# Kernel tuning notes

Hardware: AMD Instinct MI355X
Metric: run time of the kernel (lower is better)

## Reference

```python
import jax, jax.numpy as jnp
import numpy as np
import math

# dims
B, C, T, P = 32, 8, 20000, 25          # batch, emg channels, time, patch size
D, H, M, NL = 512, 8, 256, 2            # d_model, heads, random features, layers
FFN, NC, HID = 1024, 10, 128            # ffn hidden, num classes, pool hidden
DH = D // H                             # d_head
EPS_LN = 1e-5


def _sample_omega(d, m, rng):
    # Orthogonal Random Features: blocks of QR(G) rows scaled by chi(d) norms
    blocks = []
    for _ in range(math.ceil(m / d)):
        G = rng.standard_normal((d, d)).astype(np.float32)
        Q, _ = np.linalg.qr(G)
        S = Q * np.linalg.norm(G, axis=1, keepdims=True)
        blocks.append(S.T)
    return np.concatenate(blocks, axis=1)[:, :m]


def setup_inputs() -> dict:
    key = jax.random.key(0)
    ks = jax.random.split(key, 16)
    rng = np.random.default_rng(0)
    s = 0.02
    f32 = jnp.float32
    return {
        "x": jax.random.normal(ks[0], (B, C, T), f32),
        "patch_W": jax.random.normal(ks[1], (C * P, D), f32) * s,
        "patch_b": jnp.zeros((D,), f32),
        "patch_g": jnp.ones((D,), f32),
        "patch_beta": jnp.zeros((D,), f32),
        "ln1_g": jnp.ones((NL, D), f32),
        "ln1_b": jnp.zeros((NL, D), f32),
        "qW": jax.random.normal(ks[2], (NL, D, D), f32) * s,
        "kW": jax.random.normal(ks[3], (NL, D, D), f32) * s,
        "vW": jax.random.normal(ks[4], (NL, D, D), f32) * s,
        "oW": jax.random.normal(ks[5], (NL, D, D), f32) * s,
        "ob": jnp.zeros((NL, D), f32),
        "omega": jnp.stack([jnp.asarray(_sample_omega(DH, M, rng)) for _ in range(NL)]),
        "ln2_g": jnp.ones((NL, D), f32),
        "ln2_b": jnp.zeros((NL, D), f32),
        "f1W": jax.random.normal(ks[6], (NL, D, FFN), f32) * s,
        "f1b": jnp.zeros((NL, FFN), f32),
        "f2W": jax.random.normal(ks[7], (NL, FFN, D), f32) * s,
        "f2b": jnp.zeros((NL, D), f32),
        "poolW1": jax.random.normal(ks[8], (D, HID), f32) * s,
        "poolW2": jax.random.normal(ks[9], (HID, 1), f32) * s,
        "headW": jax.random.normal(ks[10], (2 * D, NC), f32) * s,
        "headb": jnp.zeros((NC,), f32),
    }


def _ln(x, g, b):
    mu = jnp.mean(x, -1, keepdims=True)
    v = jnp.mean((x - mu) ** 2, -1, keepdims=True)
    return (x - mu) / jnp.sqrt(v + EPS_LN) * g + b


def _phi(x, omega):
    # FAVOR+ positive feature map: exp(x'w / d^{1/4} - |x|^2/(2 sqrt(d))) / sqrt(m)
    xs = x / (DH ** 0.25)                               # (B,H,L,d)
    proj = jnp.einsum('bhld,dm->bhlm', xs, omega)       # (B,H,L,m)
    nsq = 0.5 * jnp.sum(xs * xs, -1, keepdims=True)
    return jnp.exp(proj - nsq) / (M ** 0.5)


def _attn(x, qW, kW, vW, oW, ob, omega):
    Bx, L, _ = x.shape
    Q = (x @ qW).reshape(Bx, L, H, DH).transpose(0, 2, 1, 3)
    K = (x @ kW).reshape(Bx, L, H, DH).transpose(0, 2, 1, 3)
    V = (x @ vW).reshape(Bx, L, H, DH).transpose(0, 2, 1, 3)
    Qf = _phi(Q, omega)
    Kf = _phi(K, omega)
    KV = jnp.einsum('bhlm,bhld->bhmd', Kf, V)           # O(L m d)
    out = jnp.einsum('bhlm,bhmd->bhld', Qf, KV)
    norm = jnp.einsum('bhlm,bhm->bhl', Qf, Kf.sum(2))[..., None]
    out = out / jnp.maximum(norm, 1e-6)
    out = out.transpose(0, 2, 1, 3).reshape(Bx, L, D)
    return out @ oW + ob


def _forward(x, patch_W, patch_b, patch_g, patch_beta, ln1_g, ln1_b, qW, kW, vW,
             oW, ob, omega, ln2_g, ln2_b, f1W, f1b, f2W, f2b, poolW1, poolW2,
             headW, headb):
    Bx, Cx, Tx = x.shape
    pad = (-Tx) % P
    if pad:
        x = jnp.pad(x, ((0, 0), (0, 0), (0, pad)))
    L = x.shape[2] // P
    # patchify: (B,C,T)->(B,L,C*P) then linear + LN
    tok = x.reshape(Bx, Cx, L, P).transpose(0, 2, 1, 3).reshape(Bx, L, Cx * P)
    h = _ln(tok @ patch_W + patch_b, patch_g, patch_beta)
    for l in range(NL):  # pre-LN performer layers (dropout = eval mode)
        h = h + _attn(_ln(h, ln1_g[l], ln1_b[l]), qW[l], kW[l], vW[l], oW[l], ob[l], omega[l])
        z = _ln(h, ln2_g[l], ln2_b[l])
        h = h + (jax.nn.gelu(z @ f1W[l] + f1b[l], approximate=False) @ f2W[l] + f2b[l])
    # attentive statistics pooling over tokens
    alpha = jax.nn.softmax(jnp.tanh(h @ poolW1) @ poolW2, axis=1)  # (B,L,1)
    mu = jnp.sum(alpha * h, axis=1)
    var = jnp.sum(alpha * h * h, axis=1) - mu * mu
    feat = jnp.concatenate([mu, jnp.sqrt(jnp.clip(var, 1e-8))], axis=1)
    return feat @ headW + headb  # (B, NC)


def reference(x, patch_W, patch_b, patch_g, patch_beta, ln1_g, ln1_b, qW, kW, vW,
              oW, ob, omega, ln2_g, ln2_b, f1W, f1b, f2W, f2b, poolW1, poolW2,
              headW, headb):
    return _forward(x, patch_W, patch_b, patch_g, patch_beta, ln1_g, ln1_b, qW,
                    kW, vW, oW, ob, omega, ln2_g, ln2_b, f1W, f1b, f2W, f2b,
                    poolW1, poolW2, headW, headb)
```

## Files before the change

kernel.cpp:

```cpp
#include <hip/hip_runtime.h>
#include <math.h>

#define BB 32
#define CC 8
#define TT 20000
#define PP 25
#define LL 800
#define CP 200
#define DD 512
#define HH 8
#define MM 256
#define NLAYER 2
#define DHH 64
#define FF 1024
#define NCLS 10
#define HIDP 128
#define BL (BB*LL)
#define KPATCH 256

#define WT_PATCH 0
#define WT_QKV0  131072
#define WT_OW0   917504
#define WT_F10   1179648
#define WT_F20   1703936
#define WT_QKV1  2228224
#define WT_OW1   3014656
#define WT_F11   3276800
#define WT_F21   3801088
#define WT_POOL  4325376
#define WT_TOTAL 4390912
#define NUC 5120

typedef unsigned short u16;
typedef unsigned int u32;
typedef __attribute__((ext_vector_type(8))) short short8;
typedef __attribute__((ext_vector_type(4))) float f32x4;

__device__ __forceinline__ float b2f(u16 v) { return __uint_as_float(((u32)v) << 16); }
__device__ __forceinline__ float b2f_lo(u32 u) { return __uint_as_float(u << 16); }
__device__ __forceinline__ float b2f_hi(u32 u) { return __uint_as_float(u & 0xFFFF0000u); }
__device__ __forceinline__ u16 f2b(float f) {
  u32 u = __float_as_uint(f);
  u32 r = u + 0x7FFFu + ((u >> 16) & 1u);
  return (u16)(r >> 16);
}
__device__ __forceinline__ float ldx(const void* p, size_t i, int flag) {
  return flag ? b2f(((const u16*)p)[i]) : ((const float*)p)[i];
}
typedef const __attribute__((address_space(1))) u32 gas_u32;
typedef __attribute__((address_space(3))) u32 las_u32;
__device__ __forceinline__ void gload16(const void* g, void* l) {
  __builtin_amdgcn_global_load_lds((gas_u32*)(size_t)g, (las_u32*)(size_t)l, 16, 0, 0);
}

__global__ void sniff_kernel(const u32* __restrict__ g, u32* __restrict__ flagp) {
  if (threadIdx.x == 0) flagp[0] = (g[0] == 0x3F800000u) ? 0u : 1u;
}

__global__ void sentinel_kernel(u16* out, int n) {
  int i = blockIdx.x * 256 + threadIdx.x;
  if (i < n) out[i] = f2b(1.0e9f);
}

__global__ void patchify_kernel(const void* __restrict__ x, u16* __restrict__ tok,
                                const u32* __restrict__ dflag) {
  int flag = (int)dflag[0];
  int idx = blockIdx.x * 256 + threadIdx.x;
  if (idx >= BL * KPATCH) return;
  int col = idx & (KPATCH - 1), row = idx >> 8;
  if (col >= CP) { tok[idx] = 0; return; }
  int b = row / LL, l = row % LL;
  int c = col / PP, p = col % PP;
  tok[idx] = f2b(ldx(x, ((size_t)b * CC + c) * TT + l * PP + p, flag));
}

__global__ void omcvt_kernel(const void* __restrict__ om, u16* __restrict__ ombT,
                             const u32* __restrict__ dflag) {
  int flag = (int)dflag[0];
  const float inv4 = 0.35355339059327373f;
  int idx = blockIdx.x * 256 + threadIdx.x;
  if (idx >= NLAYER * MM * DHH) return;
  int l = idx >> 14;
  int r = idx & (MM * DHH - 1);
  int feat = r >> 6, k = r & 63;
  ombT[idx] = f2b(inv4 * ldx(om, (size_t)l * DHH * MM + (size_t)k * MM + feat, flag));
}

struct Seg { int t0, wsel, gsel, woff, goff, wtoff, ucoff, K, N, Kp; };
__constant__ Seg g_segs[14] = {
  {   0, 0, -1,      0,   0, WT_PATCH,          -1,  200,  512,  256},
  {  32, 2,  0,      0,   0, WT_QKV0,             0,  512,  512,  512},
  {  96, 3,  0,      0,   0, WT_QKV0 + 262144,  512,  512,  512,  512},
  { 160, 1,  0,      0,   0, WT_QKV0 + 524288, 1024,  512,  512,  512},
  { 224, 4, -1,      0,   0, WT_OW0,            -1,  512,  512,  512},
  { 288, 5,  1,      0,   0, WT_F10,           1536,  512, 1024,  512},
  { 416, 6, -1,      0,   0, WT_F20,            -1, 1024,  512, 1024},
  { 544, 2,  0, 262144, 512, WT_QKV1,          2560,  512,  512,  512},
  { 608, 3,  0, 262144, 512, WT_QKV1 + 262144, 3072,  512,  512,  512},
  { 672, 1,  0, 262144, 512, WT_QKV1 + 524288, 3584,  512,  512,  512},
  { 736, 4, -1, 262144,   0, WT_OW1,            -1,  512,  512,  512},
  { 800, 5,  1, 524288, 512, WT_F11,           4096,  512, 1024,  512},
  { 928, 6, -1, 524288,   0, WT_F21,            -1, 1024,  512, 1024},
  {1056, 7, -1,      0,   0, WT_POOL,           -1,  512,  128,  512},
};

__global__ __launch_bounds__(256) void megawt_kernel(
    const void* __restrict__ patchW, const void* __restrict__ qW,
    const void* __restrict__ kW, const void* __restrict__ vW,
    const void* __restrict__ oW, const void* __restrict__ f1W,
    const void* __restrict__ f2W, const void* __restrict__ poolW1,
    const void* __restrict__ ln1g, const void* __restrict__ ln1b,
    const void* __restrict__ ln2g, const void* __restrict__ ln2b,
    u16* __restrict__ wtall, float* __restrict__ pU, float* __restrict__ pC,
    const u32* __restrict__ dflag) {
  int flag = (int)dflag[0];
  int bid = blockIdx.x;
  int si = 0;
#pragma unroll
  for (int i = 1; i < 14; i++) if (bid >= g_segs[i].t0) si = i;
  Seg sg = g_segs[si];
  const void* W = (sg.wsel == 0) ? patchW : (sg.wsel == 1) ? qW : (sg.wsel == 2) ? kW
               : (sg.wsel == 3) ? vW : (sg.wsel == 4) ? oW : (sg.wsel == 5) ? f1W
               : (sg.wsel == 6) ? f2W : poolW1;
  const void* gv = (sg.gsel == 0) ? ln1g : (sg.gsel == 1) ? ln2g : nullptr;
  const void* bv = (sg.gsel == 0) ? ln1b : (sg.gsel == 1) ? ln2b : nullptr;
  int lt = bid - sg.t0;
  int nx = sg.N >> 6;
  int n0 = (lt % nx) * 64, k0 = (lt / nx) * 64;
  bool hasU = sg.ucoff >= 0;

  __shared__ float tile[64][65];
  __shared__ float sU[4][64], sC[4][64];
  int tn = threadIdx.x & 63;
  int tk = threadIdx.x >> 6;
  float su = 0.f, sc = 0.f;
#pragma unroll 4
  for (int i = 0; i < 16; i++) {
    int k = k0 + tk * 16 + i;
    float gw = 0.f;
    if (k < sg.K) {
      float w = ldx(W, (size_t)sg.woff + (size_t)k * sg.N + n0 + tn, flag);
      float g = gv ? ldx(gv, (size_t)sg.goff + k, flag) : 1.0f;
      gw = g * w;
      if (hasU) {
        su += gw;
        sc = fmaf(ldx(bv, (size_t)sg.goff + k, flag), w, sc);
      }
    }
    tile[tk * 16 + i][tn] = gw;
  }
  if (hasU) { sU[tk][tn] = su; sC[tk][tn] = sc; }
  __syncthreads();
  if (hasU && tk == 0) {
    pU[(size_t)(k0 >> 6) * NUC + sg.ucoff + n0 + tn] =
        sU[0][tn] + sU[1][tn] + sU[2][tn] + sU[3][tn];
    pC[(size_t)(k0 >> 6) * NUC + sg.ucoff + n0 + tn] =
        sC[0][tn] + sC[1][tn] + sC[2][tn] + sC[3][tn];
  }
#pragma unroll 4
  for (int i = 0; i < 16; i++) {
    int n = n0 + tk * 16 + i;
    wtall[(size_t)sg.wtoff + (size_t)n * sg.Kp + k0 + tn] = f2b(tile[tn][tk * 16 + i]);
  }
}

__global__ __launch_bounds__(256) void ucr_kernel(const float* __restrict__ pU,
    const float* __restrict__ pC, float* __restrict__ u, float* __restrict__ c, int N) {
  int n = blockIdx.x * 256 + threadIdx.x;
  if (n >= N) return;
  float su = 0.f, sc = 0.f;
#pragma unroll
  for (int ky = 0; ky < 8; ky++) {
    su += pU[(size_t)ky * N + n];
    sc += pC[(size_t)ky * N + n];
  }
  u[n] = su;
  c[n] = sc;
}

template<int ACT, bool HAS_BIAS, bool HAS_RES, int LNE, bool SPLIT3, bool STATS>
__global__ __launch_bounds__(256, 4) void mgemm(
    const u16* __restrict__ A, const u16* __restrict__ Wt,
    const void* __restrict__ bias, size_t biasoff,
    const float* __restrict__ stA, const float* __restrict__ stB,
    const float* __restrict__ uvec, const float* __restrict__ cvec,
    const u16* res, u16* out, u16* out2, u16* out3,
    float* __restrict__ oSum, float* __restrict__ oSsq,
    int Kp, int N, const u32* __restrict__ dflag) {
  const int flag = (int)dflag[0];
  alignas(16) __shared__ u16 smem[128 * 128];
  __shared__ float statL[256];
  u16* As = smem;
  u16* Bs = smem + 128 * 64;
  int tid = threadIdx.x;
  int flat = blockIdx.y * gridDim.x + blockIdx.x;
  int xcd = flat & 7;
  int p_ = flat >> 3;
  int gx = gridDim.x;
  int mtile = xcd * (gridDim.y >> 3) + p_ / gx;
  int ntile = p_ % gx;
  int m0 = mtile * 128, n0 = ntile * 128;
  int wid = tid >> 6, lane = tid & 63;
  int wm = (wid >> 1) * 64, wn = (wid & 1) * 64;
  int quad = lane >> 4, cl = lane & 15;

  if (LNE == 1) {
    if (tid < 128) {
      statL[tid] = stA[m0 + tid];
      statL[128 + tid] = stB[m0 + tid];
    }
  } else if (LNE == 2) {
    if (tid < 128) {
      float s = 0.f, q = 0.f;
#pragma unroll
      for (int s8 = 0; s8 < 8; s8++) {
        s += stA[(size_t)s8 * BL + m0 + tid];
        q += stB[(size_t)s8 * BL + m0 + tid];
      }
      float mu = s * (1.f / DD);
      float var = q * (1.f / DD) - mu * mu;
      statL[tid] = mu;
      statL[128 + tid] = 1.0f / sqrtf(var + 1e-5f);
    }
  }

  f32x4 acc[4][4] = {};
  int r_ = tid >> 3, c_ = tid & 7;
  for (int k0 = 0; k0 < Kp; k0 += 64) {
    __syncthreads();
#pragma unroll
    for (int p = 0; p < 4; p++) {
      int row = p * 32 + r_;
      int gc = (c_ ^ (row & 7)) * 8;
      int lbase = ((p * 256 + (tid & ~63)) * 8);
      gload16(A + (size_t)(m0 + row) * Kp + k0 + gc, &As[lbase]);
      gload16(Wt + (size_t)(n0 + row) * Kp + k0 + gc, &Bs[lbase]);
    }
    __syncthreads();
#pragma unroll
    for (int kk = 0; kk < 64; kk += 32) {
      int qb = (kk >> 3) + quad;
      short8 af[4], bf[4];
#pragma unroll
      for (int mt = 0; mt < 4; mt++) {
        int arow = wm + mt * 16 + cl;
        af[mt] = *(const short8*)(&As[(arow * 8 + (qb ^ (cl & 7))) * 8]);
      }
#pragma unroll
      for (int nt = 0; nt < 4; nt++) {
        int brow = wn + nt * 16 + cl;
        bf[nt] = *(const short8*)(&Bs[(brow * 8 + (qb ^ (cl & 7))) * 8]);
      }
#pragma unroll
      for (int mt = 0; mt < 4; mt++)
#pragma unroll
        for (int nt = 0; nt < 4; nt++)
          acc[mt][nt] = __builtin_amdgcn_mfma_f32_16x16x32_bf16(
              af[mt], bf[nt], acc[mt][nt], 0, 0, 0);
    }
  }
  __syncthreads();
  u16* Cs = smem;
  float sA[4][4] = {}, qA[4][4] = {};
#pragma unroll
  for (int nt = 0; nt < 4; nt++) {
    int tcol = wn + nt * 16 + cl;
    int gcol = n0 + tcol;
    float bvv = HAS_BIAS ? ldx(bias, biasoff + gcol, flag) : 0.f;
    float uv_ = 0.f, cv_ = 0.f;
    if (LNE) { uv_ = uvec[gcol]; cv_ = cvec[gcol]; }
#pragma unroll
    for (int mt = 0; mt < 4; mt++) {
#pragma unroll
      for (int r = 0; r < 4; r++) {
        int trow = wm + mt * 16 + quad * 4 + r;
        int grow = m0 + trow;
        float v = acc[mt][nt][r];
        if (LNE) {
          float rv_ = statL[128 + trow];
          v = rv_ * v - rv_ * statL[trow] * uv_ + cv_;
        }
        v += bvv;
        if (ACT == 1) v = 0.5f * v * (1.0f + erff(v * 0.7071067811865476f));
        else if (ACT == 2) v = tanhf(v);
        if (HAS_RES) v += b2f(res[(size_t)grow * N + gcol]);
        u16 wv = f2b(v);
        Cs[trow * 128 + tcol] = wv;
        if (STATS) {
          float vr = b2f(wv);
          sA[mt][r] += vr;
          qA[mt][r] += vr * vr;
        }
      }
    }
  }
  if (STATS) {
#pragma unroll
    for (int mt = 0; mt < 4; mt++)
#pragma unroll
      for (int r = 0; r < 4; r++) {
        float s = sA[mt][r], q = qA[mt][r];
        s += __shfl_xor(s, 1, 64); s += __shfl_xor(s, 2, 64);
        s += __shfl_xor(s, 4, 64); s += __shfl_xor(s, 8, 64);
        q += __shfl_xor(q, 1, 64); q += __shfl_xor(q, 2, 64);
        q += __shfl_xor(q, 4, 64); q += __shfl_xor(q, 8, 64);
        if (cl == 0) {
          int grow = m0 + wm + mt * 16 + quad * 4 + r;
          int slot = ntile * 2 + (wid & 1);
          oSum[(size_t)slot * BL + grow] = s;
          oSsq[(size_t)slot * BL + grow] = q;
        }
      }
  }
  __syncthreads();
  {
    u16* dstbuf;
    int colbase, stride;
    if (SPLIT3) {
      int sel = n0 >> 9;
      dstbuf = (sel == 0) ? out : (sel == 1) ? out2 : out3;
      colbase = n0 & 511;
      stride = 512;
    } else {
      dstbuf = out;
      colbase = n0;
      stride = N;
    }
    int c8 = (tid & 15) * 8, rb = tid >> 4;
#pragma unroll
    for (int i = 0; i < 8; i++) {
      int trow = i * 16 + rb;
      uint4 vv = *(const uint4*)(&Cs[trow * 128 + c8]);
      *(uint4*)(&dstbuf[(size_t)(m0 + trow) * stride + colbase + c8]) = vv;
    }
  }
}

__global__ __launch_bounds__(256) void ln_apply_kernel(const u16* __restrict__ x,
    const float* __restrict__ pSum, const float* __restrict__ pSsq,
    const void* __restrict__ g, const void* __restrict__ b, u16* __restrict__ out,
    float* __restrict__ muv, float* __restrict__ rinvv,
    const u32* __restrict__ dflag) {
  int flag = (int)dflag[0];
  int row = blockIdx.x * 4 + (threadIdx.x >> 6);
  int lane = threadIdx.x & 63;
  float s = 0.f, q = 0.f;
#pragma unroll
  for (int s8 = 0; s8 < 8; s8++) {
    s += pSum[(size_t)s8 * BL + row];
    q += pSsq[(size_t)s8 * BL + row];
  }
  float m = s * (1.f / DD);
  float var = q * (1.f / DD) - m * m;
  float rvv = 1.0f / sqrtf(var + 1e-5f);

  const u16* xr = x + (size_t)row * DD + lane * 8;
  uint4 u = *(const uint4*)xr;
  float f[8] = {b2f_lo(u.x), b2f_hi(u.x), b2f_lo(u.y), b2f_hi(u.y),
                b2f_lo(u.z), b2f_hi(u.z), b2f_lo(u.w), b2f_hi(u.w)};
  u16 r[8];
  float os = 0.f, oq = 0.f;
#pragma unroll
  for (int j = 0; j < 8; j++) {
    float gg = ldx(g, lane * 8 + j, flag);
    float bb = ldx(b, lane * 8 + j, flag);
    r[j] = f2b((f[j] - m) * rvv * gg + bb);
    float hv = b2f(r[j]);
    os += hv;
    oq = fmaf(hv, hv, oq);
  }
  uint4 pr;
  pr.x = (u32)r[0] | ((u32)r[1] << 16);
  pr.y = (u32)r[2] | ((u32)r[3] << 16);
  pr.z = (u32)r[4] | ((u32)r[5] << 16);
  pr.w = (u32)r[6] | ((u32)r[7] << 16);
  *(uint4*)(out + (size_t)row * DD + lane * 8) = pr;
#pragma unroll
  for (int o = 1; o < 64; o <<= 1) {
    os += __shfl_xor(os, o, 64);
    oq += __shfl_xor(oq, o, 64);
  }
  if (lane == 0) {
    float mo = os * (1.f / DD);
    float vo = oq * (1.f / DD) - mo * mo;
    muv[row] = mo;
    rinvv[row] = 1.0f / sqrtf(vo + 1e-5f);
  }
}

__global__ __launch_bounds__(256) void kv_kernel_mfma(
    const u16* __restrict__ Kb, const u16* __restrict__ Vb,
    const u16* __restrict__ omt, u16* __restrict__ KVT_g) {
  int bh = blockIdx.x; int b = bh >> 3, h = bh & 7;
  int tid = threadIdx.x;
  int wid = tid >> 6, lane = tid & 63;
  int quad = lane >> 4, cl = lane & 15;
  __shared__ u16 VT[80 * 40];
  __shared__ u16 KfT[256 * 40];

  short8 omB[4][2];
#pragma unroll
  for (int nt = 0; nt < 4; nt++)
#pragma unroll
    for (int ks = 0; ks < 2; ks++)
      omB[nt][ks] = *(const short8*)(omt + (size_t)(wid * 64 + nt * 16 + cl) * 64
                                         + ks * 32 + quad * 8);
  for (int e = tid; e < 512; e += 256)
    VT[(64 + (e >> 5)) * 40 + (e & 31)] = ((e >> 5) == 0) ? (u16)0x3F80 : (u16)0;

  f32x4 acc2[4][5] = {};

  for (int l0 = 0; l0 < LL; l0 += 32) {
    __syncthreads();
#pragma unroll
    for (int i = 0; i < 4; i++) {
      int idx = tid + i * 256;
      int rr = idx >> 5, pp = idx & 31;
      u32 uv = *(const u32*)(Vb + ((size_t)(b * LL + l0 + rr)) * DD + h * DHH + pp * 2);
      VT[(pp * 2) * 40 + rr] = (u16)(uv & 0xFFFF);
      VT[(pp * 2 + 1) * 40 + rr] = (u16)(uv >> 16);
    }
    short8 aK[2][2];
    float nsk[2];
#pragma unroll
    for (int mt = 0; mt < 2; mt++) {
      const u16* ksrc = Kb + ((size_t)(b * LL + l0 + mt * 16 + cl)) * DD + h * DHH;
#pragma unroll
      for (int ks = 0; ks < 2; ks++)
        aK[mt][ks] = *(const short8*)(ksrc + ks * 32 + quad * 8);
      float q = 0.f;
#pragma unroll
      for (int ks = 0; ks < 2; ks++)
#pragma unroll
        for (int j = 0; j < 8; j++) {
          float f = b2f((u16)aK[mt][ks][j]);
          q = fmaf(f, f, q);
        }
      q += __shfl_xor(q, 16, 64);
      q += __shfl_xor(q, 32, 64);
      nsk[mt] = 0.0625f * q;
    }
    f32x4 acc1[2][4] = {};
#pragma unroll
    for (int ks = 0; ks < 2; ks++)
#pragma unroll
      for (int mt = 0; mt < 2; mt++)
#pragma unroll
        for (int nt = 0; nt < 4; nt++)
          acc1[mt][nt] = __builtin_amdgcn_mfma_f32_16x16x32_bf16(
              aK[mt][ks], omB[nt][ks], acc1[mt][nt], 0, 0, 0);
#pragma unroll
    for (int mt = 0; mt < 2; mt++) {
      f32x4 nsv;
#pragma unroll
      for (int r = 0; r < 4; r++) nsv[r] = __shfl(nsk[mt], quad * 4 + r, 64);
#pragma unroll
      for (int nt = 0; nt < 4; nt++) {
        int m = wid * 64 + nt * 16 + cl;
        u16 kf16[4];
#pragma unroll
        for (int r = 0; r < 4; r++)
          kf16[r] = f2b(__expf(acc1[mt][nt][r] - nsv[r]) * 0.0625f);
        uint2 pk;
        pk.x = (u32)kf16[0] | ((u32)kf16[1] << 16);
        pk.y = (u32)kf16[2] | ((u32)kf16[3] << 16);
        *(uint2*)(&KfT[m * 40 + mt * 16 + quad * 4]) = pk;
      }
    }
    __syncthreads();
    short8 aF[4], bV[5];
#pragma unroll
    for (int mt2 = 0; mt2 < 4; mt2++)
      aF[mt2] = *(const short8*)(&KfT[(wid * 64 + mt2 * 16 + cl) * 40 + quad * 8]);
#pragma unroll
    for (int nt2 = 0; nt2 < 5; nt2++)
      bV[nt2] = *(const short8*)(&VT[(nt2 * 16 + cl) * 40 + quad * 8]);
#pragma unroll
    for (int mt2 = 0; mt2 < 4; mt2++)
#pragma unroll
      for (int nt2 = 0; nt2 < 5; nt2++)
        acc2[mt2][nt2] = __builtin_amdgcn_mfma_f32_16x16x32_bf16(
            aF[mt2], bV[nt2], acc2[mt2][nt2], 0, 0, 0);
  }
  u16* base = KVT_g + (size_t)bh * 80 * 256;
#pragma unroll
  for (int mt2 = 0; mt2 < 4; mt2++) {
    int m0 = wid * 64 + mt2 * 16 + quad * 4;
#pragma unroll
    for (int nt2 = 0; nt2 < 4; nt2++) {
      u16 w[4];
#pragma unroll
      for (int r = 0; r < 4; r++) w[r] = f2b(acc2[mt2][nt2][r]);
      uint2 pk;
      pk.x = (u32)w[0] | ((u32)w[1] << 16);
      pk.y = (u32)w[2] | ((u32)w[3] << 16);
      *(uint2*)(&base[(size_t)(nt2 * 16 + cl) * 256 + m0]) = pk;
    }
    if (cl == 0) {
      u16 w[4];
#pragma unroll
      for (int r = 0; r < 4; r++) w[r] = f2b(acc2[mt2][4][r]);
      uint2 pk;
      pk.x = (u32)w[0] | ((u32)w[1] << 16);
      pk.y = (u32)w[2] | ((u32)w[3] << 16);
      *(uint2*)(&base[(size_t)64 * 256 + m0]) = pk;
    }
  }
}

__global__ __launch_bounds__(256) void attn_out_mfma(
    u16* __restrict__ Qb, const u16* __restrict__ KVT_g,
    const u16* __restrict__ omt) {
  int bh = blockIdx.x; int b = bh >> 3, h = bh & 7;
  int chunk = blockIdx.y;
  int tid = threadIdx.x;
  int wid = tid >> 6, lane = tid & 63;
  int quad = lane >> 4, cl = lane & 15;
  __shared__ u16 smem[64 * 264 + 80 * 264];
  u16* Qf = smem;
  u16* KVT = smem + 64 * 264;

  const u16* kvsrc = KVT_g + (size_t)bh * 80 * 256;
#pragma unroll
  for (int i = 0; i < 9; i++) {
    int idx = tid + i * 256;
    if (idx < 2080) {
      int row = idx >> 5, c8 = (idx & 31) * 8;
      *(uint4*)(&KVT[row * 264 + c8]) = *(const uint4*)(kvsrc + (size_t)row * 256 + c8);
    }
  }

  short8 omB[4][2];
#pragma unroll
  for (int nt = 0; nt < 4; nt++)
#pragma unroll
    for (int ks = 0; ks < 2; ks++)
      omB[nt][ks] = *(const short8*)(omt + (size_t)(wid * 64 + nt * 16 + cl) * 64
                                         + ks * 32 + quad * 8);

  int t0 = chunk * 64;
  short8 aQ[4][2];
  float nss[4];
#pragma unroll
  for (int mt = 0; mt < 4; mt++) {
    int tglob = t0 + mt * 16 + cl;
    int trow = tglob < LL ? tglob : LL - 1;
    const u16* qsrc = Qb + ((size_t)(b * LL + trow)) * DD + h * DHH;
#pragma unroll
    for (int ks = 0; ks < 2; ks++)
      aQ[mt][ks] = *(const short8*)(qsrc + ks * 32 + quad * 8);
    float q = 0.f;
#pragma unroll
    for (int ks = 0; ks < 2; ks++)
#pragma unroll
      for (int j = 0; j < 8; j++) {
        float f = b2f((u16)aQ[mt][ks][j]);
        q = fmaf(f, f, q);
      }
    q += __shfl_xor(q, 16, 64);
    q += __shfl_xor(q, 32, 64);
    nss[mt] = 0.0625f * q;
  }

  f32x4 acc1[4][4] = {};
#pragma unroll
  for (int ks = 0; ks < 2; ks++)
#pragma unroll
    for (int mt = 0; mt < 4; mt++)
#pragma unroll
      for (int nt = 0; nt < 4; nt++)
        acc1[mt][nt] = __builtin_amdgcn_mfma_f32_16x16x32_bf16(
            omB[nt][ks], aQ[mt][ks], acc1[mt][nt], 0, 0, 0);
#pragma unroll
  for (int mt = 0; mt < 4; mt++) {
#pragma unroll
    for (int nt = 0; nt < 4; nt++) {
      u16 w[4];
#pragma unroll
      for (int r = 0; r < 4; r++)
        w[r] = f2b(__expf(acc1[mt][nt][r] - nss[mt]) * 0.0625f);
      uint2 pk;
      pk.x = (u32)w[0] | ((u32)w[1] << 16);
      pk.y = (u32)w[2] | ((u32)w[3] << 16);
      *(uint2*)(&Qf[(mt * 16 + cl) * 264 + wid * 64 + nt * 16 + quad * 4]) = pk;
    }
  }
  __syncthreads();
  f32x4 acc2[5] = {};
#pragma unroll
  for (int ks2 = 0; ks2 < 8; ks2++) {
    short8 aF = *(const short8*)(&Qf[(wid * 16 + cl) * 264 + ks2 * 32 + quad * 8]);
#pragma unroll
    for (int nt2 = 0; nt2 < 5; nt2++) {
      short8 bK = *(const short8*)(&KVT[(nt2 * 16 + cl) * 264 + ks2 * 32 + quad * 8]);
      acc2[nt2] = __builtin_amdgcn_mfma_f32_16x16x32_bf16(bK, aF, acc2[nt2], 0, 0, 0);
    }
  }
  float nval = __shfl(acc2[4][0], cl, 64);
  float inv = 1.0f / fmaxf(nval, 1e-6f);
  int tglob = t0 + wid * 16 + cl;
  if (tglob < LL) {
    u16* dst = Qb + ((size_t)(b * LL + tglob)) * DD + h * DHH;
#pragma unroll
    for (int nt2 = 0; nt2 < 4; nt2++) {
      u16 w[4];
#pragma unroll
      for (int r = 0; r < 4; r++) w[r] = f2b(acc2[nt2][r] * inv);
      uint2 pk;
      pk.x = (u32)w[0] | ((u32)w[1] << 16);
      pk.y = (u32)w[2] | ((u32)w[3] << 16);
      *(uint2*)(dst + nt2 * 16 + quad * 4) = pk;
    }
  }
}

__global__ __launch_bounds__(256) void score_kernel(const u16* __restrict__ t,
    const void* __restrict__ w2, float* __restrict__ sc, const u32* __restrict__ dflag) {
  int flag = (int)dflag[0];
  int row = blockIdx.x * 4 + (threadIdx.x >> 6);
  int lane = threadIdx.x & 63;
  const u16* tr = t + (size_t)row * HIDP;
  float p = b2f(tr[lane]) * ldx(w2, lane, flag) +
            b2f(tr[lane + 64]) * ldx(w2, lane + 64, flag);
#pragma unroll
  for (int o = 32; o; o >>= 1) p += __shfl_down(p, o, 64);
  if (lane == 0) sc[row] = p;
}

__global__ __launch_bounds__(256) void softmax_kernel(const float* __restrict__ sc,
    float* __restrict__ alpha) {
  __shared__ float sm[4];
  int b = blockIdx.x, tid = threadIdx.x;
  float mx = -1e30f;
  for (int i = tid; i < LL; i += 256) mx = fmaxf(mx, sc[b * LL + i]);
#pragma unroll
  for (int o = 32; o; o >>= 1) mx = fmaxf(mx, __shfl_down(mx, o, 64));
  if ((tid & 63) == 0) sm[tid >> 6] = mx;
  __syncthreads();
  mx = fmaxf(fmaxf(sm[0], sm[1]), fmaxf(sm[2], sm[3]));
  float s = 0.f;
  for (int i = tid; i < LL; i += 256) {
    float e = expf(sc[b * LL + i] - mx);
    alpha[b * LL + i] = e;
    s += e;
  }
  __syncthreads();
#pragma unroll
  for (int o = 32; o; o >>= 1) s += __shfl_down(s, o, 64);
  if ((tid & 63) == 0) sm[tid >> 6] = s;
  __syncthreads();
  float invs = 1.f / (sm[0] + sm[1] + sm[2] + sm[3]);
  for (int i = tid; i < LL; i += 256) alpha[b * LL + i] *= invs;
}

__global__ __launch_bounds__(512) void pool_stats_kernel(const u16* __restrict__ h,
    const float* __restrict__ alpha, float* __restrict__ feat) {
  int b = blockIdx.x, d = threadIdx.x;
  float mu = 0.f, m2 = 0.f;
  const u16* hb = h + (size_t)b * LL * DD + d;
  const float* ab = alpha + b * LL;
  for (int l = 0; l < LL; l++) {
    float a = ab[l], v = b2f(hb[(size_t)l * DD]);
    mu = fmaf(a, v, mu);
    m2 = fmaf(a * v, v, m2);
  }
  feat[b * 2 * DD + d] = mu;
  float var = m2 - mu * mu;
  feat[b * 2 * DD + DD + d] = sqrtf(fmaxf(var, 1e-8f));
}

__global__ __launch_bounds__(320) void head_kernel(const float* __restrict__ feat,
    const void* __restrict__ hw, const void* __restrict__ hb, void* out,
    const u32* __restrict__ dflag) {
  int flag = (int)dflag[0];
  int b = blockIdx.x;
  int t = threadIdx.x;
  int n = t >> 5, j0 = t & 31;
  float p = 0.f;
  for (int j = j0; j < 2 * DD; j += 32)
    p = fmaf(feat[b * 2 * DD + j], ldx(hw, (size_t)j * NCLS + n, flag), p);
#pragma unroll
  for (int o = 16; o; o >>= 1) p += __shfl_down(p, o, 32);
  if (j0 == 0) {
    float v = p + ldx(hb, n, flag);
    if (flag) ((u16*)out)[b * NCLS + n] = f2b(v);
    else ((float*)out)[b * NCLS + n] = v;
  }
}

extern "C" void kernel_launch(void* const* d_in, const int* in_sizes, int n_in,
                              void* d_out, int out_size, void* d_ws, size_t ws_size,
                              hipStream_t stream) {
  char* ws = (char*)d_ws;
  size_t off = 0;
  auto alloc = [&](size_t bytes) -> char* {
    char* p = ws + off;
    off += (bytes + 255) & ~(size_t)255;
    return p;
  };
  u16* hbuf = (u16*)alloc((size_t)BL * DD * 2);
  u16* buf1 = (u16*)alloc((size_t)BL * DD * 2);
  u16* buf2 = (u16*)alloc((size_t)BL * DD * 2);
  u16* KVT_g = (u16*)alloc((size_t)BB * HH * 80 * 256 * 2);
  float* muv = (float*)alloc((size_t)BL * 4);
  float* rinvv = (float*)alloc((size_t)BL * 4);
  float* scores = (float*)alloc((size_t)BL * 4);
  float* alpha = (float*)alloc((size_t)BL * 4);
  float* feat = (float*)alloc((size_t)BB * 2 * DD * 4);
  float* uvec = (float*)alloc((size_t)NUC * 4);
  float* cvec = (float*)alloc((size_t)NUC * 4);
  float* pU = (float*)alloc((size_t)8 * NUC * 4);
  float* pC = (float*)alloc((size_t)8 * NUC * 4);
  float* pSum = (float*)alloc((size_t)8 * BL * 4);
  float* pSsq = (float*)alloc((size_t)8 * BL * 4);
  u16* ombT = (u16*)alloc((size_t)NLAYER * MM * DHH * 2);
  u16* wtall = (u16*)alloc((size_t)WT_TOTAL * 2);
  u32* dflag = (u32*)alloc(256);
  size_t off_base = off;
  u16* bufQ = (u16*)alloc((size_t)BL * DD * 2);
  size_t off_full = off;

  if (ws_size < off_base) {
    sentinel_kernel<<<2, 256, 0, stream>>>((u16*)d_out, out_size);
    return;
  }
  const bool fused = (ws_size >= off_full);

  const void* x       = d_in[0];
  const void* patchW  = d_in[1];
  const void* patchb  = d_in[2];
  const void* patchg  = d_in[3];
  const void* patchbe = d_in[4];
  const void* ln1g    = d_in[5];
  const void* ln1b    = d_in[6];
  const void* qW      = d_in[7];
  const void* kW      = d_in[8];
  const void* vW      = d_in[9];
  const void* oW      = d_in[10];
  const void* ob      = d_in[11];
  const void* omg     = d_in[12];
  const void* ln2g    = d_in[13];
  const void* ln2b    = d_in[14];
  const void* f1W     = d_in[15];
  const void* f1b     = d_in[16];
  const void* f2W     = d_in[17];
  const void* f2b_    = d_in[18];
  const void* poolW1  = d_in[19];
  const void* poolW2  = d_in[20];
  const void* headW   = d_in[21];
  const void* headb   = d_in[22];

  sniff_kernel<<<1, 64, 0, stream>>>((const u32*)patchg, dflag);

  patchify_kernel<<<(BL * KPATCH) / 256, 256, 0, stream>>>(x, buf1, dflag);
  omcvt_kernel<<<(NLAYER * MM * DHH + 255) / 256, 256, 0, stream>>>(omg, ombT, dflag);
  megawt_kernel<<<1072, 256, 0, stream>>>(patchW, qW, kW, vW, oW, f1W, f2W, poolW1,
                                          ln1g, ln1b, ln2g, ln2b, wtall, pU, pC, dflag);
  ucr_kernel<<<NUC / 256, 256, 0, stream>>>(pU, pC, uvec, cvec, NUC);

  mgemm<0, true, false, 0, false, true><<<dim3(4, 200), 256, 0, stream>>>(
      buf1, wtall + WT_PATCH, patchb, 0, nullptr, nullptr, nullptr, nullptr,
      nullptr, buf2, nullptr, nullptr, pSum, pSsq, KPATCH, DD, dflag);
  ln_apply_kernel<<<BL / 4, 256, 0, stream>>>(buf2, pSum, pSsq, patchg, patchbe,
                                              hbuf, muv, rinvv, dflag);

  for (int l = 0; l < NLAYER; l++) {
    size_t oD = (size_t)l * DD;
    size_t oF = (size_t)l * FF;
    const u16* omtl = ombT + (size_t)l * MM * DHH;
    const u16* qkvT = wtall + (l == 0 ? WT_QKV0 : WT_QKV1);
    const u16* oWT  = wtall + (l == 0 ? WT_OW0 : WT_OW1);
    const u16* f1T  = wtall + (l == 0 ? WT_F10 : WT_F11);
    const u16* f2T  = wtall + (l == 0 ? WT_F20 : WT_F21);
    const float* uq = uvec + (l == 0 ? 0 : 2560);
    const float* cq = cvec + (l == 0 ? 0 : 2560);
    const float* uf = uvec + (l == 0 ? 1536 : 4096);
    const float* cf = cvec + (l == 0 ? 1536 : 4096);

    u16* qb;
    if (fused) {
      if (l == 0)
        mgemm<0, false, false, 1, true, false><<<dim3(12, 200), 256, 0, stream>>>(
            hbuf, qkvT, nullptr, 0, muv, rinvv, uq, cq, nullptr,
            buf1, buf2, bufQ, nullptr, nullptr, DD, 3 * DD, dflag);
      else
        mgemm<0, false, false, 2, true, false><<<dim3(12, 200), 256, 0, stream>>>(
            hbuf, qkvT, nullptr, 0, pSum, pSsq, uq, cq, nullptr,
            buf1, buf2, bufQ, nullptr, nullptr, DD, 3 * DD, dflag);
      kv_kernel_mfma<<<BB * HH, 256, 0, stream>>>(buf1, buf2, omtl, KVT_g);
      qb = bufQ;
    } else {
      if (l == 0) {
        mgemm<0, false, false, 1, false, false><<<dim3(4, 200), 256, 0, stream>>>(
            hbuf, qkvT, nullptr, 0, muv, rinvv, uq, cq, nullptr,
            buf1, nullptr, nullptr, nullptr, nullptr, DD, DD, dflag);
        mgemm<0, false, false, 1, false, false><<<dim3(4, 200), 256, 0, stream>>>(
            hbuf, qkvT + 262144, nullptr, 0, muv, rinvv, uq + 512, cq + 512, nullptr,
            buf2, nullptr, nullptr, nullptr, nullptr, DD, DD, dflag);
      } else {
        mgemm<0, false, false, 2, false, false><<<dim3(4, 200), 256, 0, stream>>>(
            hbuf, qkvT, nullptr, 0, pSum, pSsq, uq, cq, nullptr,
            buf1, nullptr, nullptr, nullptr, nullptr, DD, DD, dflag);
        mgemm<0, false, false, 2, false, false><<<dim3(4, 200), 256, 0, stream>>>(
            hbuf, qkvT + 262144, nullptr, 0, pSum, pSsq, uq + 512, cq + 512, nullptr,
            buf2, nullptr, nullptr, nullptr, nullptr, DD, DD, dflag);
      }
      kv_kernel_mfma<<<BB * HH, 256, 0, stream>>>(buf1, buf2, omtl, KVT_g);
      if (l == 0)
        mgemm<0, false, false, 1, false, false><<<dim3(4, 200), 256, 0, stream>>>(
            hbuf, qkvT + 524288, nullptr, 0, muv, rinvv, uq + 1024, cq + 1024, nullptr,
            buf1, nullptr, nullptr, nullptr, nullptr, DD, DD, dflag);
      else
        mgemm<0, false, false, 2, false, false><<<dim3(4, 200), 256, 0, stream>>>(
            hbuf, qkvT + 524288, nullptr, 0, pSum, pSsq, uq + 1024, cq + 1024, nullptr,
            buf1, nullptr, nullptr, nullptr, nullptr, DD, DD, dflag);
      qb = buf1;
    }
    attn_out_mfma<<<dim3(BB * HH, 13), 256, 0, stream>>>(qb, KVT_g, omtl);
    mgemm<0, true, true, 0, false, true><<<dim3(4, 200), 256, 0, stream>>>(
        qb, oWT, ob, oD, nullptr, nullptr, nullptr, nullptr,
        hbuf, hbuf, nullptr, nullptr, pSum, pSsq, DD, DD, dflag);
    mgemm<1, true, false, 2, false, false><<<dim3(8, 200), 256, 0, stream>>>(
        hbuf, f1T, f1b, oF, pSum, pSsq, uf, cf, nullptr,
        buf1, nullptr, nullptr, nullptr, nullptr, DD, FF, dflag);
    if (l == 0)
      mgemm<0, true, true, 0, false, true><<<dim3(4, 200), 256, 0, stream>>>(
          buf1, f2T, f2b_, oD, nullptr, nullptr, nullptr, nullptr,
          hbuf, hbuf, nullptr, nullptr, pSum, pSsq, FF, DD, dflag);
    else
      mgemm<0, true, true, 0, false, false><<<dim3(4, 200), 256, 0, stream>>>(
          buf1, f2T, f2b_, oD, nullptr, nullptr, nullptr, nullptr,
          hbuf, hbuf, nullptr, nullptr, nullptr, nullptr, FF, DD, dflag);
  }

  mgemm<2, false, false, 0, false, false><<<dim3(1, 200), 256, 0, stream>>>(
      hbuf, wtall + WT_POOL, nullptr, 0, nullptr, nullptr, nullptr, nullptr,
      nullptr, buf1, nullptr, nullptr, nullptr, nullptr, DD, HIDP, dflag);
  score_kernel<<<BL / 4, 256, 0, stream>>>(buf1, poolW2, scores, dflag);
  softmax_kernel<<<BB, 256, 0, stream>>>(scores, alpha);
  pool_stats_kernel<<<BB, 512, 0, stream>>>(hbuf, alpha, feat);
  head_kernel<<<BB, 320, 0, stream>>>(feat, headW, headb, d_out, dflag);
}
```

Before: 904.3 us.

## Merge prep kernels, prefetch V in kv kernel, split pooling, coarsen attn_out

Folds the patchify, omega conversion and weight prep kernels into a single launch to cut launch overhead. The kv kernel now register-prefetches the next V tile so the global load overlaps the MFMA work. attn_out processes two 64-token chunks per block, launching 7 y-blocks instead of 13. Pooling statistics are split across 8 segments per batch and then reduced, so many more blocks run than the previous 32. Together these trade a few extra registers and one extra tiny kernel for more parallelism and fewer launches.

```diff
diff --git a/kernel.cpp b/kernel.cpp
--- a/kernel.cpp
+++ b/kernel.cpp
@@ -31,6 +31,10 @@
 #define WT_TOTAL 4390912
 #define NUC 5120
 
+#define PREP_MEGA 1072
+#define PREP_OM   1200
+#define PREP_TOT  26800
+
 typedef unsigned short u16;
 typedef unsigned int u32;
 typedef __attribute__((ext_vector_type(8))) short short8;
@@ -60,30 +64,6 @@
 __global__ void sentinel_kernel(u16* out, int n) {
   int i = blockIdx.x * 256 + threadIdx.x;
   if (i < n) out[i] = f2b(1.0e9f);
-}
-
-__global__ void patchify_kernel(const void* __restrict__ x, u16* __restrict__ tok,
-                                const u32* __restrict__ dflag) {
-  int flag = (int)dflag[0];
-  int idx = blockIdx.x * 256 + threadIdx.x;
-  if (idx >= BL * KPATCH) return;
-  int col = idx & (KPATCH - 1), row = idx >> 8;
-  if (col >= CP) { tok[idx] = 0; return; }
-  int b = row / LL, l = row % LL;
-  int c = col / PP, p = col % PP;
-  tok[idx] = f2b(ldx(x, ((size_t)b * CC + c) * TT + l * PP + p, flag));
-}
-
-__global__ void omcvt_kernel(const void* __restrict__ om, u16* __restrict__ ombT,
-                             const u32* __restrict__ dflag) {
-  int flag = (int)dflag[0];
-  const float inv4 = 0.35355339059327373f;
-  int idx = blockIdx.x * 256 + threadIdx.x;
-  if (idx >= NLAYER * MM * DHH) return;
-  int l = idx >> 14;
-  int r = idx & (MM * DHH - 1);
-  int feat = r >> 6, k = r & 63;
-  ombT[idx] = f2b(inv4 * ldx(om, (size_t)l * DHH * MM + (size_t)k * MM + feat, flag));
 }
 
 struct Seg { int t0, wsel, gsel, woff, goff, wtoff, ucoff, K, N, Kp; };
@@ -104,17 +84,37 @@
   {1056, 7, -1,      0,   0, WT_POOL,           -1,  512,  128,  512},
 };
 
-__global__ __launch_bounds__(256) void megawt_kernel(
+__global__ __launch_bounds__(256) void prep_kernel(
     const void* __restrict__ patchW, const void* __restrict__ qW,
     const void* __restrict__ kW, const void* __restrict__ vW,
     const void* __restrict__ oW, const void* __restrict__ f1W,
     const void* __restrict__ f2W, const void* __restrict__ poolW1,
     const void* __restrict__ ln1g, const void* __restrict__ ln1b,
     const void* __restrict__ ln2g, const void* __restrict__ ln2b,
+    const void* __restrict__ om, const void* __restrict__ x,
     u16* __restrict__ wtall, float* __restrict__ pU, float* __restrict__ pC,
+    u16* __restrict__ ombT, u16* __restrict__ tok,
     const u32* __restrict__ dflag) {
   int flag = (int)dflag[0];
   int bid = blockIdx.x;
+  if (bid >= PREP_OM) {
+    int idx = (bid - PREP_OM) * 256 + threadIdx.x;
+    int col = idx & (KPATCH - 1), row = idx >> 8;
+    if (col >= CP) { tok[idx] = 0; return; }
+    int b = row / LL, l = row % LL;
+    int c = col / PP, p = col % PP;
+    tok[idx] = f2b(ldx(x, ((size_t)b * CC + c) * TT + l * PP + p, flag));
+    return;
+  }
+  if (bid >= PREP_MEGA) {
+    const float inv4 = 0.35355339059327373f;
+    int idx = (bid - PREP_MEGA) * 256 + threadIdx.x;
+    int l = idx >> 14;
+    int r = idx & (MM * DHH - 1);
+    int feat = r >> 6, k = r & 63;
+    ombT[idx] = f2b(inv4 * ldx(om, (size_t)l * DHH * MM + (size_t)k * MM + feat, flag));
+    return;
+  }
   int si = 0;
 #pragma unroll
   for (int i = 1; i < 14; i++) if (bid >= g_segs[i].t0) si = i;
@@ -408,6 +408,16 @@
   for (int e = tid; e < 512; e += 256)
     VT[(64 + (e >> 5)) * 40 + (e & 31)] = ((e >> 5) == 0) ? (u16)0x3F80 : (u16)0;
 
+  int rr_ = (tid * 4) >> 7;
+  (void)rr_;
+  u32 vreg[4];
+#pragma unroll
+  for (int i = 0; i < 4; i++) {
+    int idx = tid + i * 256;
+    int rr = idx >> 5, pp = idx & 31;
+    vreg[i] = *(const u32*)(Vb + ((size_t)(b * LL + rr)) * DD + h * DHH + pp * 2);
+  }
+
   f32x4 acc2[4][5] = {};
 
   for (int l0 = 0; l0 < LL; l0 += 32) {
@@ -416,9 +426,17 @@
     for (int i = 0; i < 4; i++) {
       int idx = tid + i * 256;
       int rr = idx >> 5, pp = idx & 31;
-      u32 uv = *(const u32*)(Vb + ((size_t)(b * LL + l0 + rr)) * DD + h * DHH + pp * 2);
+      u32 uv = vreg[i];
       VT[(pp * 2) * 40 + rr] = (u16)(uv & 0xFFFF);
       VT[(pp * 2 + 1) * 40 + rr] = (u16)(uv >> 16);
+    }
+    if (l0 + 32 < LL) {
+#pragma unroll
+      for (int i = 0; i < 4; i++) {
+        int idx = tid + i * 256;
+        int rr = idx >> 5, pp = idx & 31;
+        vreg[i] = *(const u32*)(Vb + ((size_t)(b * LL + l0 + 32 + rr)) * DD + h * DHH + pp * 2);
+      }
     }
     short8 aK[2][2];
     float nsk[2];
@@ -512,7 +530,7 @@
     u16* __restrict__ Qb, const u16* __restrict__ KVT_g,
     const u16* __restrict__ omt) {
   int bh = blockIdx.x; int b = bh >> 3, h = bh & 7;
-  int chunk = blockIdx.y;
+  int cy = blockIdx.y;
   int tid = threadIdx.x;
   int wid = tid >> 6, lane = tid & 63;
   int quad = lane >> 4, cl = lane & 15;
@@ -538,79 +556,85 @@
       omB[nt][ks] = *(const short8*)(omt + (size_t)(wid * 64 + nt * 16 + cl) * 64
                                          + ks * 32 + quad * 8);
 
-  int t0 = chunk * 64;
-  short8 aQ[4][2];
-  float nss[4];
-#pragma unroll
-  for (int mt = 0; mt < 4; mt++) {
-    int tglob = t0 + mt * 16 + cl;
-    int trow = tglob < LL ? tglob : LL - 1;
-    const u16* qsrc = Qb + ((size_t)(b * LL + trow)) * DD + h * DHH;
+#pragma unroll
+  for (int s = 0; s < 2; s++) {
+    int chunk = cy * 2 + s;
+    if (chunk >= 13) break;
+    int t0 = chunk * 64;
+    short8 aQ[4][2];
+    float nss[4];
+#pragma unroll
+    for (int mt = 0; mt < 4; mt++) {
+      int tglob = t0 + mt * 16 + cl;
+      int trow = tglob < LL ? tglob : LL - 1;
+      const u16* qsrc = Qb + ((size_t)(b * LL + trow)) * DD + h * DHH;
+#pragma unroll
+      for (int ks = 0; ks < 2; ks++)
+        aQ[mt][ks] = *(const short8*)(qsrc + ks * 32 + quad * 8);
+      float q = 0.f;
+#pragma unroll
+      for (int ks = 0; ks < 2; ks++)
+#pragma unroll
+        for (int j = 0; j < 8; j++) {
+          float f = b2f((u16)aQ[mt][ks][j]);
+          q = fmaf(f, f, q);
+        }
+      q += __shfl_xor(q, 16, 64);
+      q += __shfl_xor(q, 32, 64);
+      nss[mt] = 0.0625f * q;
+    }
+
+    f32x4 acc1[4][4] = {};
 #pragma unroll
     for (int ks = 0; ks < 2; ks++)
-      aQ[mt][ks] = *(const short8*)(qsrc + ks * 32 + quad * 8);
-    float q = 0.f;
-#pragma unroll
-    for (int ks = 0; ks < 2; ks++)
-#pragma unroll
-      for (int j = 0; j < 8; j++) {
-        float f = b2f((u16)aQ[mt][ks][j]);
-        q = fmaf(f, f, q);
-      }
-    q += __shfl_xor(q, 16, 64);
-    q += __shfl_xor(q, 32, 64);
-    nss[mt] = 0.0625f * q;
-  }
-
-  f32x4 acc1[4][4] = {};
-#pragma unroll
-  for (int ks = 0; ks < 2; ks++)
-#pragma unroll
-    for (int mt = 0; mt < 4; mt++)
-#pragma unroll
-      for (int nt = 0; nt < 4; nt++)
-        acc1[mt][nt] = __builtin_amdgcn_mfma_f32_16x16x32_bf16(
-            omB[nt][ks], aQ[mt][ks], acc1[mt][nt], 0, 0, 0);
-#pragma unroll
-  for (int mt = 0; mt < 4; mt++) {
-#pragma unroll
-    for (int nt = 0; nt < 4; nt++) {
-      u16 w[4];
-#pragma unroll
-      for (int r = 0; r < 4; r++)
-        w[r] = f2b(__expf(acc1[mt][nt][r] - nss[mt]) * 0.0625f);
-      uint2 pk;
-      pk.x = (u32)w[0] | ((u32)w[1] << 16);
-      pk.y = (u32)w[2] | ((u32)w[3] << 16);
-      *(uint2*)(&Qf[(mt * 16 + cl) * 264 + wid * 64 + nt * 16 + quad * 4]) = pk;
-    }
-  }
-  __syncthreads();
-  f32x4 acc2[5] = {};
-#pragma unroll
-  for (int ks2 = 0; ks2 < 8; ks2++) {
-    short8 aF = *(const short8*)(&Qf[(wid * 16 + cl) * 264 + ks2 * 32 + quad * 8]);
-#pragma unroll
-    for (int nt2 = 0; nt2 < 5; nt2++) {
-      short8 bK = *(const short8*)(&KVT[(nt2 * 16 + cl) * 264 + ks2 * 32 + quad * 8]);
-      acc2[nt2] = __builtin_amdgcn_mfma_f32_16x16x32_bf16(bK, aF, acc2[nt2], 0, 0, 0);
-    }
-  }
-  float nval = __shfl(acc2[4][0], cl, 64);
-  float inv = 1.0f / fmaxf(nval, 1e-6f);
-  int tglob = t0 + wid * 16 + cl;
-  if (tglob < LL) {
-    u16* dst = Qb + ((size_t)(b * LL + tglob)) * DD + h * DHH;
-#pragma unroll
-    for (int nt2 = 0; nt2 < 4; nt2++) {
-      u16 w[4];
-#pragma unroll
-      for (int r = 0; r < 4; r++) w[r] = f2b(acc2[nt2][r] * inv);
-      uint2 pk;
-      pk.x = (u32)w[0] | ((u32)w[1] << 16);
-      pk.y = (u32)w[2] | ((u32)w[3] << 16);
-      *(uint2*)(dst + nt2 * 16 + quad * 4) = pk;
-    }
+#pragma unroll
+      for (int mt = 0; mt < 4; mt++)
+#pragma unroll
+        for (int nt = 0; nt < 4; nt++)
+          acc1[mt][nt] = __builtin_amdgcn_mfma_f32_16x16x32_bf16(
+              omB[nt][ks], aQ[mt][ks], acc1[mt][nt], 0, 0, 0);
+#pragma unroll
+    for (int mt = 0; mt < 4; mt++) {
+#pragma unroll
+      for (int nt = 0; nt < 4; nt++) {
+        u16 w[4];
+#pragma unroll
+        for (int r = 0; r < 4; r++)
+          w[r] = f2b(__expf(acc1[mt][nt][r] - nss[mt]) * 0.0625f);
+        uint2 pk;
+        pk.x = (u32)w[0] | ((u32)w[1] << 16);
+        pk.y = (u32)w[2] | ((u32)w[3] << 16);
+        *(uint2*)(&Qf[(mt * 16 + cl) * 264 + wid * 64 + nt * 16 + quad * 4]) = pk;
+      }
+    }
+    __syncthreads();
+    f32x4 acc2[5] = {};
+#pragma unroll
+    for (int ks2 = 0; ks2 < 8; ks2++) {
+      short8 aF = *(const short8*)(&Qf[(wid * 16 + cl) * 264 + ks2 * 32 + quad * 8]);
+#pragma unroll
+      for (int nt2 = 0; nt2 < 5; nt2++) {
+        short8 bK = *(const short8*)(&KVT[(nt2 * 16 + cl) * 264 + ks2 * 32 + quad * 8]);
+        acc2[nt2] = __builtin_amdgcn_mfma_f32_16x16x32_bf16(bK, aF, acc2[nt2], 0, 0, 0);
+      }
+    }
+    float nval = __shfl(acc2[4][0], cl, 64);
+    float inv = 1.0f / fmaxf(nval, 1e-6f);
+    int tglob = t0 + wid * 16 + cl;
+    if (tglob < LL) {
+      u16* dst = Qb + ((size_t)(b * LL + tglob)) * DD + h * DHH;
+#pragma unroll
+      for (int nt2 = 0; nt2 < 4; nt2++) {
+        u16 w[4];
+#pragma unroll
+        for (int r = 0; r < 4; r++) w[r] = f2b(acc2[nt2][r] * inv);
+        uint2 pk;
+        pk.x = (u32)w[0] | ((u32)w[1] << 16);
+        pk.y = (u32)w[2] | ((u32)w[3] << 16);
+        *(uint2*)(dst + nt2 * 16 + quad * 4) = pk;
+      }
+    }
+    if (s == 0) __syncthreads();
   }
 }
 
@@ -653,20 +677,32 @@
   for (int i = tid; i < LL; i += 256) alpha[b * LL + i] *= invs;
 }
 
-__global__ __launch_bounds__(512) void pool_stats_kernel(const u16* __restrict__ h,
-    const float* __restrict__ alpha, float* __restrict__ feat) {
-  int b = blockIdx.x, d = threadIdx.x;
+__global__ __launch_bounds__(512) void pool_part_kernel(const u16* __restrict__ h,
+    const float* __restrict__ alpha, float* __restrict__ pmu, float* __restrict__ pm2) {
+  int b = blockIdx.x, seg = blockIdx.y, d = threadIdx.x;
+  const u16* hb = h + (size_t)b * LL * DD + (size_t)seg * 100 * DD + d;
+  const float* ab = alpha + b * LL + seg * 100;
   float mu = 0.f, m2 = 0.f;
-  const u16* hb = h + (size_t)b * LL * DD + d;
-  const float* ab = alpha + b * LL;
-  for (int l = 0; l < LL; l++) {
+  for (int l = 0; l < 100; l++) {
     float a = ab[l], v = b2f(hb[(size_t)l * DD]);
     mu = fmaf(a, v, mu);
     m2 = fmaf(a * v, v, m2);
   }
+  pmu[((size_t)seg * BB + b) * DD + d] = mu;
+  pm2[((size_t)seg * BB + b) * DD + d] = m2;
+}
+
+__global__ __launch_bounds__(512) void pool_reduce_kernel(const float* __restrict__ pmu,
+    const float* __restrict__ pm2, float* __restrict__ feat) {
+  int b = blockIdx.x, d = threadIdx.x;
+  float mu = 0.f, m2 = 0.f;
+#pragma unroll
+  for (int s = 0; s < 8; s++) {
+    mu += pmu[((size_t)s * BB + b) * DD + d];
+    m2 += pm2[((size_t)s * BB + b) * DD + d];
+  }
   feat[b * 2 * DD + d] = mu;
-  float var = m2 - mu * mu;
-  feat[b * 2 * DD + DD + d] = sqrtf(fmaxf(var, 1e-8f));
+  feat[b * 2 * DD + DD + d] = sqrtf(fmaxf(m2 - mu * mu, 1e-8f));
 }
 
 __global__ __launch_bounds__(320) void head_kernel(const float* __restrict__ feat,
@@ -752,10 +788,9 @@
 
   sniff_kernel<<<1, 64, 0, stream>>>((const u32*)patchg, dflag);
 
-  patchify_kernel<<<(BL * KPATCH) / 256, 256, 0, stream>>>(x, buf1, dflag);
-  omcvt_kernel<<<(NLAYER * MM * DHH + 255) / 256, 256, 0, stream>>>(omg, ombT, dflag);
-  megawt_kernel<<<1072, 256, 0, stream>>>(patchW, qW, kW, vW, oW, f1W, f2W, poolW1,
-                                          ln1g, ln1b, ln2g, ln2b, wtall, pU, pC, dflag);
+  prep_kernel<<<PREP_TOT, 256, 0, stream>>>(patchW, qW, kW, vW, oW, f1W, f2W, poolW1,
+                                            ln1g, ln1b, ln2g, ln2b, omg, x,
+                                            wtall, pU, pC, ombT, buf1, dflag);
   ucr_kernel<<<NUC / 256, 256, 0, stream>>>(pU, pC, uvec, cvec, NUC);
 
   mgemm<0, true, false, 0, false, true><<<dim3(4, 200), 256, 0, stream>>>(
@@ -816,7 +851,7 @@
             buf1, nullptr, nullptr, nullptr, nullptr, DD, DD, dflag);
       qb = buf1;
     }
-    attn_out_mfma<<<dim3(BB * HH, 13), 256, 0, stream>>>(qb, KVT_g, omtl);
+    attn_out_mfma<<<dim3(BB * HH, 7), 256, 0, stream>>>(qb, KVT_g, omtl);
     mgemm<0, true, true, 0, false, true><<<dim3(4, 200), 256, 0, stream>>>(
         qb, oWT, ob, oD, nullptr, nullptr, nullptr, nullptr,
         hbuf, hbuf, nullptr, nullptr, pSum, pSsq, DD, DD, dflag);
@@ -838,6 +873,7 @@
       nullptr, buf1, nullptr, nullptr, nullptr, nullptr, DD, HIDP, dflag);
   score_kernel<<<BL / 4, 256, 0, stream>>>(buf1, poolW2, scores, dflag);
   softmax_kernel<<<BB, 256, 0, stream>>>(scores, alpha);
-  pool_stats_kernel<<<BB, 512, 0, stream>>>(hbuf, alpha, feat);
+  pool_part_kernel<<<dim3(BB, 8), 512, 0, stream>>>(hbuf, alpha, pSum, pSsq);
+  pool_reduce_kernel<<<BB, 512, 0, stream>>>(pSum, pSsq, feat);
   head_kernel<<<BB, 320, 0, stream>>>(feat, headW, headb, d_out, dflag);
 }
```

After: 1.019 ms. 12.7% more time.
